# Performance work log

Measured on AMD Instinct MI355X. Metric: run time of the kernel, lower is better.

The kernel has to match this reference:

```python
import jax, jax.numpy as jnp
import numpy as np

FIELD_DIMS = [100000, 50000, 20000, 10000, 5000, 2000, 1000, 500, 100, 10]
FACTOR_DIM = 8
BATCH = 16384
NUM_FIELDS = len(FIELD_DIMS)
INPUT_DIM = int(sum(FIELD_DIMS))
OFFSETS = np.concatenate([[0], np.cumsum(FIELD_DIMS)[:-1]]).astype(np.int32)


def setup_inputs() -> dict:
    key = jax.random.key(0)
    k_x, k_w, k_e = jax.random.split(key, 3)
    # per-field indices, each column in [0, field_dims[f])
    cols = [jax.random.randint(jax.random.fold_in(k_x, f), (BATCH,), 0, d, dtype=jnp.int32)
            for f, d in enumerate(FIELD_DIMS)]
    x = jnp.stack(cols, axis=1)  # (B, F) int32
    # linear: weight (input_dim,), bias scalar (nn.Linear(input_dim, 1))
    w_linear = jax.random.normal(k_w, (INPUT_DIM,), dtype=jnp.float32) * 0.01
    b_linear = jnp.zeros((), dtype=jnp.float32)
    # one embedding table per field: (F, input_dim, D)
    emb = jax.random.normal(k_e, (NUM_FIELDS, INPUT_DIM, FACTOR_DIM), dtype=jnp.float32) * 0.01
    return {"x": x, "w_linear": w_linear, "b_linear": b_linear, "emb": emb}


def reference(x, w_linear, b_linear, emb):
    # x: (B, F) int32 per-field raw indices
    F = emb.shape[0]
    x_off = x + jnp.asarray(OFFSETS, x.dtype)[None, :]  # (B, F) global indices
    # Linear term: scatter-to-onehot + matmul == gather weights and sum
    # (indices are distinct per sample since fields occupy disjoint ranges)
    y_lin = jnp.take(w_linear, x_off, axis=0).sum(axis=1) + b_linear  # (B,)
    # FFM term: all_emb[f, b, g, d] = emb[f, x_off[b, g], d]
    all_emb = jnp.take(emb, x_off, axis=1)          # (F, B, F, D)
    A = jnp.transpose(all_emb, (0, 2, 1, 3))        # (F, F, B, D): A[f, g] = emb_f(x_g)
    prod = (A * jnp.transpose(A, (1, 0, 2, 3))).sum(-1)  # (F, F, B): <emb_f(x_g), emb_g(x_f)>
    mask = jnp.triu(jnp.ones((F, F), prod.dtype), k=1)   # pairs f < g
    y_ffm = (prod * mask[:, :, None]).sum((0, 1))   # (B,)
    return y_lin + y_ffm
```

## Files before the change

### kernel.cpp

```cpp
#include <hip/hip_runtime.h>

#define NUM_FIELDS 10
#define FACTOR_DIM 8
#define BATCH      16384
#define INPUT_DIM  188610
#define NPAIRS     45

__device__ __constant__ int c_off[NUM_FIELDS] =
    {0, 100000, 150000, 170000, 180000, 185000, 187000, 188000, 188500, 188600};

__device__ __constant__ int c_pf[NPAIRS] = {
    0,0,0,0,0,0,0,0,0,
    1,1,1,1,1,1,1,1,
    2,2,2,2,2,2,2,
    3,3,3,3,3,3,
    4,4,4,4,4,
    5,5,5,5,
    6,6,6,
    7,7,
    8};
__device__ __constant__ int c_pg[NPAIRS] = {
    1,2,3,4,5,6,7,8,9,
    2,3,4,5,6,7,8,9,
    3,4,5,6,7,8,9,
    4,5,6,7,8,9,
    5,6,7,8,9,
    6,7,8,9,
    7,8,9,
    8,9,
    9};

__global__ __launch_bounds__(256) void ffm_kernel(
    const int* __restrict__ x,
    const float* __restrict__ w,
    const float* __restrict__ blin,
    const float* __restrict__ emb,
    float* __restrict__ out)
{
    const int gtid   = blockIdx.x * blockDim.x + threadIdx.x;
    const int wave   = gtid >> 6;
    const int lane   = threadIdx.x & 63;
    const int nwaves = (gridDim.x * blockDim.x) >> 6;

    const float bl = *blin;

    const int p  = (lane < NPAIRS) ? lane : 0;
    const int pf = c_pf[p];
    const int pg = c_pg[p];
    const int jl = (lane >= NPAIRS && lane < NPAIRS + NUM_FIELDS) ? (lane - NPAIRS) : 0;

    for (int b = wave; b < BATCH; b += nwaves) {
        int idx = 0;
        if (lane < NUM_FIELDS) idx = x[b * NUM_FIELDS + lane] + c_off[lane];

        const int idx_g = __shfl(idx, pg);
        const int idx_f = __shfl(idx, pf);
        const int idx_j = __shfl(idx, jl);

        float val = 0.0f;
        if (lane < NPAIRS) {
            const float4* pa = reinterpret_cast<const float4*>(
                emb + ((size_t)pf * INPUT_DIM + idx_g) * FACTOR_DIM);
            const float4* pb = reinterpret_cast<const float4*>(
                emb + ((size_t)pg * INPUT_DIM + idx_f) * FACTOR_DIM);
            float4 a0 = pa[0], a1 = pa[1];
            float4 b0 = pb[0], b1 = pb[1];
            val = a0.x * b0.x + a0.y * b0.y + a0.z * b0.z + a0.w * b0.w
                + a1.x * b1.x + a1.y * b1.y + a1.z * b1.z + a1.w * b1.w;
        } else if (lane < NPAIRS + NUM_FIELDS) {
            val = w[idx_j];
        }

        #pragma unroll
        for (int m = 1; m < 64; m <<= 1)
            val += __shfl_xor(val, m);

        if (lane == 0) out[b] = val + bl;
    }
}

extern "C" void kernel_launch(void* const* d_in, const int* in_sizes, int n_in,
                              void* d_out, int out_size, void* d_ws, size_t ws_size,
                              hipStream_t stream) {
    const int*   x    = (const int*)d_in[0];
    const float* w    = (const float*)d_in[1];
    const float* blin = (const float*)d_in[2];
    const float* emb  = (const float*)d_in[3];
    float*       out  = (float*)d_out;

    dim3 block(256);
    dim3 grid(2048);
    hipLaunchKernelGGL(ffm_kernel, grid, block, 0, stream, x, w, blin, emb, out);
}
```

Measured before the change: 105.3 us.

## Process four samples per wave with batched gathers before reductions

Each wave now handles four consecutive samples. It loads their 40 indices in one coalesced read and issues all embedding and weight gathers for the four samples before doing any reduction, then writes the four outputs with a single float4 store. The grid is resized to one wave per four samples, replacing the grid-stride loop. The intent is to raise memory-level parallelism and hide gather latency, at the cost of more registers per thread and fewer total waves in flight.

```diff
diff --git a/kernel.cpp b/kernel.cpp
--- a/kernel.cpp
+++ b/kernel.cpp
@@ -5,9 +5,13 @@
 #define BATCH      16384
 #define INPUT_DIM  188610
 #define NPAIRS     45
+#define SPW        4
 
-__device__ __constant__ int c_off[NUM_FIELDS] =
-    {0, 100000, 150000, 170000, 180000, 185000, 187000, 188000, 188500, 188600};
+__device__ __constant__ int c_off40[SPW * NUM_FIELDS] = {
+    0, 100000, 150000, 170000, 180000, 185000, 187000, 188000, 188500, 188600,
+    0, 100000, 150000, 170000, 180000, 185000, 187000, 188000, 188500, 188600,
+    0, 100000, 150000, 170000, 180000, 185000, 187000, 188000, 188500, 188600,
+    0, 100000, 150000, 170000, 180000, 185000, 187000, 188000, 188500, 188600};
 
 __device__ __constant__ int c_pf[NPAIRS] = {
     0,0,0,0,0,0,0,0,0,
@@ -37,10 +41,12 @@
     const float* __restrict__ emb,
     float* __restrict__ out)
 {
-    const int gtid   = blockIdx.x * blockDim.x + threadIdx.x;
-    const int wave   = gtid >> 6;
-    const int lane   = threadIdx.x & 63;
-    const int nwaves = (gridDim.x * blockDim.x) >> 6;
+    const int gtid = blockIdx.x * blockDim.x + threadIdx.x;
+    const int wave = gtid >> 6;
+    const int lane = threadIdx.x & 63;
+
+    const int b0 = wave * SPW;
+    if (b0 >= BATCH) return;
 
     const float bl = *blin;
 
@@ -49,33 +55,53 @@
     const int pg = c_pg[p];
     const int jl = (lane >= NPAIRS && lane < NPAIRS + NUM_FIELDS) ? (lane - NPAIRS) : 0;
 
-    for (int b = wave; b < BATCH; b += nwaves) {
-        int idx = 0;
-        if (lane < NUM_FIELDS) idx = x[b * NUM_FIELDS + lane] + c_off[lane];
+    int idx = 0;
+    if (lane < SPW * NUM_FIELDS)
+        idx = x[b0 * NUM_FIELDS + lane] + c_off40[lane];
 
-        const int idx_g = __shfl(idx, pg);
-        const int idx_f = __shfl(idx, pf);
-        const int idx_j = __shfl(idx, jl);
-
-        float val = 0.0f;
+    float4 va0[SPW], va1[SPW], vb0[SPW], vb1[SPW];
+    float  wv[SPW];
+    #pragma unroll
+    for (int s = 0; s < SPW; ++s) {
+        const int ig = __shfl(idx, s * NUM_FIELDS + pg);
+        const int If = __shfl(idx, s * NUM_FIELDS + pf);
+        const int ij = __shfl(idx, s * NUM_FIELDS + jl);
         if (lane < NPAIRS) {
             const float4* pa = reinterpret_cast<const float4*>(
-                emb + ((size_t)pf * INPUT_DIM + idx_g) * FACTOR_DIM);
+                emb + ((size_t)pf * INPUT_DIM + ig) * FACTOR_DIM);
             const float4* pb = reinterpret_cast<const float4*>(
-                emb + ((size_t)pg * INPUT_DIM + idx_f) * FACTOR_DIM);
-            float4 a0 = pa[0], a1 = pa[1];
-            float4 b0 = pb[0], b1 = pb[1];
-            val = a0.x * b0.x + a0.y * b0.y + a0.z * b0.z + a0.w * b0.w
-                + a1.x * b1.x + a1.y * b1.y + a1.z * b1.z + a1.w * b1.w;
+                emb + ((size_t)pg * INPUT_DIM + If) * FACTOR_DIM);
+            va0[s] = pa[0]; va1[s] = pa[1];
+            vb0[s] = pb[0]; vb1[s] = pb[1];
+            wv[s] = 0.0f;
         } else if (lane < NPAIRS + NUM_FIELDS) {
-            val = w[idx_j];
+            wv[s] = w[ij];
+        } else {
+            wv[s] = 0.0f;
         }
+    }
 
+    float res[SPW];
+    #pragma unroll
+    for (int s = 0; s < SPW; ++s) {
+        float v;
+        if (lane < NPAIRS) {
+            v = va0[s].x * vb0[s].x + va0[s].y * vb0[s].y
+              + va0[s].z * vb0[s].z + va0[s].w * vb0[s].w
+              + va1[s].x * vb1[s].x + va1[s].y * vb1[s].y
+              + va1[s].z * vb1[s].z + va1[s].w * vb1[s].w;
+        } else {
+            v = wv[s];
+        }
         #pragma unroll
         for (int m = 1; m < 64; m <<= 1)
-            val += __shfl_xor(val, m);
+            v += __shfl_xor(v, m);
+        res[s] = v;
+    }
 
-        if (lane == 0) out[b] = val + bl;
+    if (lane == 0) {
+        float4 o = make_float4(res[0] + bl, res[1] + bl, res[2] + bl, res[3] + bl);
+        *reinterpret_cast<float4*>(out + b0) = o;
     }
 }
 
@@ -89,6 +115,6 @@
     float*       out  = (float*)d_out;
 
     dim3 block(256);
-    dim3 grid(2048);
+    dim3 grid((BATCH / SPW + 3) / 4);
     hipLaunchKernelGGL(ffm_kernel, grid, block, 0, stream, x, w, blin, emb, out);
 }
```

Result: no change. 103.9 us (-1.3%).
